# Kernel tuning notes

Hardware: AMD Instinct MI355X
Metric: run time of the kernel (lower is better)

## Reference

```python
import jax, jax.numpy as jnp
import numpy as np

EMB = 512      # emb_s * head_cnt = 64 * 8
EMB_S = 64     # scale uses sqrt(emb_s), not sqrt(emb) (quirk of source)
FF = 4 * EMB
LN_EPS = 1e-5


def layer_norm(x, g, b):
    mu = jnp.mean(x, axis=-1, keepdims=True)
    var = jnp.var(x, axis=-1, keepdims=True)
    return (x - mu) * jax.lax.rsqrt(var + LN_EPS) * g + b


def setup_inputs() -> dict:
    key = jax.random.key(0)
    ks = jax.random.split(key, 12)
    B, T = 512, 128
    s = 1.0 / np.sqrt(EMB)
    sf = 1.0 / np.sqrt(FF)
    return {
        "x": jax.random.normal(ks[0], (B, T, EMB), dtype=jnp.float32),
        "wq": jax.random.normal(ks[1], (EMB, EMB), dtype=jnp.float32) * s,
        "bq": jnp.zeros((EMB,), jnp.float32),
        "wk": jax.random.normal(ks[2], (EMB, EMB), dtype=jnp.float32) * s,
        "bk": jnp.zeros((EMB,), jnp.float32),
        "wv": jax.random.normal(ks[3], (EMB, EMB), dtype=jnp.float32) * s,
        "bv": jnp.zeros((EMB,), jnp.float32),
        "g1": jnp.ones((EMB,), jnp.float32),
        "b1": jnp.zeros((EMB,), jnp.float32),
        "g2": jnp.ones((EMB,), jnp.float32),
        "b2": jnp.zeros((EMB,), jnp.float32),
        "w1": jax.random.normal(ks[4], (EMB, FF), dtype=jnp.float32) * s,
        "bm1": jnp.zeros((FF,), jnp.float32),
        "w2": jax.random.normal(ks[5], (FF, EMB), dtype=jnp.float32) * sf,
        "bm2": jnp.zeros((EMB,), jnp.float32),
    }


def reference(x, wq, bq, wk, bk, wv, bv, g1, b1, g2, b2, w1, bm1, w2, bm2):
    B, T, E = x.shape
    # --- attention sub-block (single-head over full emb, per source forward) ---
    h = layer_norm(x, g1, b1)
    q = h @ wq + bq          # [B,T,E]
    k = h @ wk + bk
    v = h @ wv + bv
    att = jnp.einsum("bte,bse->bts", q, k) * (1.0 / np.sqrt(EMB_S))
    causal = jnp.tril(jnp.ones((T, T), dtype=bool))
    att = jnp.where(causal[None, :, :], att, -jnp.inf)
    att = jax.nn.softmax(att, axis=-1)
    y = jnp.einsum("bts,bse->bte", att, v)
    x = x + y  # note: no output projection / dropout on the forward path
    # --- MLP sub-block (dropout is identity in eval) ---
    h2 = layer_norm(x, g2, b2)
    m = jax.nn.gelu(h2 @ w1 + bm1, approximate=False) @ w2 + bm2
    return x + m
```

## Files before the change

### kernel.cpp

```cpp
#include <hip/hip_runtime.h>
#include <hip/hip_bf16.h>
#include <math.h>

typedef __attribute__((ext_vector_type(8))) short s16x8;
typedef __attribute__((ext_vector_type(4))) float f32x4;

static __device__ __forceinline__ float b2f(unsigned short u) {
    union { unsigned int u; float f; } x; x.u = ((unsigned int)u) << 16; return x.f;
}
static __device__ __forceinline__ unsigned short f2b(float f) {
    __hip_bfloat16 h = __float2bfloat16(f);
    return *reinterpret_cast<unsigned short*>(&h);
}
static __device__ __forceinline__ float gelu_fast(float x) {
    float s = x * fmaf(x * x, 0.07135481242f, 1.5957691216f);
    float e = __expf(-s);
    return x * __builtin_amdgcn_rcpf(1.0f + e);
}
static __device__ __forceinline__ void gload16(void* lds, const void* g) {
    __builtin_amdgcn_global_load_lds(
        (const __attribute__((address_space(1))) unsigned int*)g,
        (__attribute__((address_space(3))) unsigned int*)lds, 16, 0, 0);
}

__global__ __launch_bounds__(256) void cvt_t_kernel(
    const float* __restrict__ W, unsigned short* __restrict__ Wt, int K, int N)
{
    __shared__ unsigned short tile[32][33];
    int n0 = blockIdx.x * 32, k0 = blockIdx.y * 32;
    int tx = threadIdx.x & 31, ty = threadIdx.x >> 5;
#pragma unroll
    for (int p = 0; p < 32; p += 8)
        tile[tx][ty + p] = f2b(W[(size_t)(k0 + ty + p) * N + n0 + tx]);
    __syncthreads();
#pragma unroll
    for (int p = 0; p < 32; p += 8)
        Wt[(size_t)(n0 + ty + p) * K + k0 + tx] = tile[ty + p][tx];
}

__global__ __launch_bounds__(256) void concat3_kernel(
    const float* __restrict__ a, const float* __restrict__ b,
    const float* __restrict__ c, float* __restrict__ o)
{
    int i = blockIdx.x * 256 + threadIdx.x;
    if (i < 512) { o[i] = a[i]; o[512 + i] = b[i]; o[1024 + i] = c[i]; }
}

__global__ __launch_bounds__(256) void ln_kernel(
    const float* __restrict__ x,
    const float* __restrict__ g,
    const float* __restrict__ b,
    unsigned short* __restrict__ out, int rows)
{
    int row  = blockIdx.x * 4 + (threadIdx.x >> 6);
    int lane = threadIdx.x & 63;
    if (row >= rows) return;
    const float* xr = x + (size_t)row * 512 + lane * 8;
    float4 d0 = *(const float4*)xr;
    float4 d1 = *(const float4*)(xr + 4);
    float v[8] = {d0.x, d0.y, d0.z, d0.w, d1.x, d1.y, d1.z, d1.w};
    float s = 0.f, ss = 0.f;
#pragma unroll
    for (int j = 0; j < 8; ++j) { s += v[j]; ss += v[j] * v[j]; }
#pragma unroll
    for (int o = 32; o > 0; o >>= 1) { s += __shfl_xor(s, o); ss += __shfl_xor(ss, o); }
    float mu   = s * (1.0f / 512.0f);
    float var  = ss * (1.0f / 512.0f) - mu * mu;
    var = fmaxf(var, 0.0f);
    float rstd = rsqrtf(var + 1e-5f);
    float4 g0 = *(const float4*)(g + lane * 8);
    float4 g1 = *(const float4*)(g + lane * 8 + 4);
    float4 b0 = *(const float4*)(b + lane * 8);
    float4 b1 = *(const float4*)(b + lane * 8 + 4);
    float gg[8] = {g0.x, g0.y, g0.z, g0.w, g1.x, g1.y, g1.z, g1.w};
    float bb[8] = {b0.x, b0.y, b0.z, b0.w, b1.x, b1.y, b1.z, b1.w};
    uint4 res; unsigned short* rs = (unsigned short*)&res;
#pragma unroll
    for (int j = 0; j < 8; ++j)
        rs[j] = f2b((v[j] - mu) * rstd * gg[j] + bb[j]);
    *(uint4*)(out + (size_t)row * 512 + lane * 8) = res;
}

__global__ __launch_bounds__(512, 4) void gemm_bt_kernel(
    const unsigned short* __restrict__ A,
    const unsigned short* __restrict__ Bt,
    const float* __restrict__ bias,
    const float* __restrict__ residual,
    void* __restrict__ Cv,
    int M, int N, int K, int act_gelu, int out_f32)
{
    __shared__ unsigned short LA[3][256][32];
    __shared__ unsigned short LB[3][128][32];

    const int tid  = threadIdx.x;
    const int w    = tid >> 6, lane = tid & 63;
    const int quad = lane >> 4, l16 = lane & 15;
    const int wm   = (w >> 1) * 64, wn = (w & 1) * 64;

    int bx = blockIdx.x, by = blockIdx.y;
    {
        int nwg = gridDim.x * gridDim.y;
        if ((nwg & 7) == 0) {
            int lid = by * gridDim.x + bx;
            int cpx = nwg >> 3;
            lid = (lid & 7) * cpx + (lid >> 3);
            bx = lid % gridDim.x;
            by = lid / gridDim.x;
        }
    }
    const int bm = by * 256, bn = bx * 128;

    const int srow = w * 16 + (lane >> 2);
    const int sg   = (lane & 3) ^ ((lane >> 3) & 3);
    const unsigned short* a_src = A  + (size_t)(bm + srow) * K + sg * 8;
    const unsigned short* b_src = Bt + (size_t)(bn + srow) * K + sg * 8;
    const size_t a_skip = (size_t)128 * K;

    const int axor = (quad ^ ((l16 >> 1) & 3)) * 8;

    f32x4 acc[4][4] = {};
    const int nt = K >> 5;

    auto STG = [&](int sb, int kt) {
        const int ko = kt << 5;
        gload16(&LA[sb][w * 16][0],       a_src + ko);
        gload16(&LA[sb][128 + w * 16][0], a_src + a_skip + ko);
        gload16(&LB[sb][w * 16][0],       b_src + ko);
    };

    STG(0, 0);
    STG(1, 1);
    asm volatile("s_waitcnt vmcnt(3)" ::: "memory");
    __builtin_amdgcn_s_barrier();

    int cur = 0, stg = 2;
    for (int t = 0; t < nt; ++t) {
        s16x8 a4[4], b4[4];
#pragma unroll
        for (int m = 0; m < 4; ++m)
            a4[m] = *(const s16x8*)&LA[cur][wm + m * 16 + l16][axor];
#pragma unroll
        for (int n = 0; n < 4; ++n)
            b4[n] = *(const s16x8*)&LB[cur][wn + n * 16 + l16][axor];

        STG(stg, (t + 2 < nt) ? t + 2 : 0);
        asm volatile("s_waitcnt vmcnt(3)" ::: "memory");
        __builtin_amdgcn_sched_barrier(0);
        __builtin_amdgcn_s_barrier();
        __builtin_amdgcn_sched_barrier(0);

        __builtin_amdgcn_s_setprio(1);
#pragma unroll
        for (int m = 0; m < 4; ++m)
#pragma unroll
            for (int n = 0; n < 4; ++n)
                acc[m][n] = __builtin_amdgcn_mfma_f32_16x16x32_bf16(a4[m], b4[n], acc[m][n], 0, 0, 0);
        __builtin_amdgcn_s_setprio(0);
        __builtin_amdgcn_sched_barrier(0);
        __builtin_amdgcn_s_barrier();

        cur = (cur == 2) ? 0 : cur + 1;
        stg = (stg == 2) ? 0 : stg + 1;
    }
    asm volatile("s_waitcnt vmcnt(0)" ::: "memory");

#pragma unroll
    for (int m = 0; m < 4; ++m) {
#pragma unroll
        for (int n = 0; n < 4; ++n) {
#pragma unroll
            for (int r = 0; r < 4; ++r) {
                int row = bm + wm + m * 16 + quad * 4 + r;
                int col = bn + wn + n * 16 + l16;
                float val = acc[m][n][r] + bias[col];
                if (act_gelu) val = gelu_fast(val);
                if (residual) val += residual[(size_t)row * N + col];
                if (out_f32) ((float*)Cv)[(size_t)row * N + col] = val;
                else ((unsigned short*)Cv)[(size_t)row * N + col] = f2b(val);
            }
        }
    }
}

__global__ __launch_bounds__(256) void attn_kernel(
    const unsigned short* __restrict__ qkv,
    const float* __restrict__ x,
    float* __restrict__ x2)
{
    __shared__ unsigned short Ps[128][128];
    __shared__ unsigned short Vs[64][128];

    int b = blockIdx.x;
    int tid = threadIdx.x;
    int wave = tid >> 6, lane = tid & 63;
    int quad = lane >> 4, l16 = lane & 15;
    const unsigned short* qb = qkv + (size_t)b * 128 * 1536;
    const size_t bo = (size_t)b * 128 * 512;

    f32x4 acc[2][8] = {};
    for (int e0 = 0; e0 < 512; e0 += 32) {
        s16x8 a0 = *(const s16x8*)(qb + (size_t)(wave * 32 + l16) * 1536 + e0 + quad * 8);
        s16x8 a1 = *(const s16x8*)(qb + (size_t)(wave * 32 + 16 + l16) * 1536 + e0 + quad * 8);
#pragma unroll
        for (int j = 0; j < 8; ++j) {
            s16x8 bf = *(const s16x8*)(qb + (size_t)(j * 16 + l16) * 1536 + 512 + e0 + quad * 8);
            acc[0][j] = __builtin_amdgcn_mfma_f32_16x16x32_bf16(a0, bf, acc[0][j], 0, 0, 0);
            acc[1][j] = __builtin_amdgcn_mfma_f32_16x16x32_bf16(a1, bf, acc[1][j], 0, 0, 0);
        }
    }

    const float NEG = -1e30f;
#pragma unroll
    for (int i = 0; i < 2; ++i) {
#pragma unroll
        for (int r = 0; r < 4; ++r) {
            int t = wave * 32 + i * 16 + quad * 4 + r;
            float m = NEG;
#pragma unroll
            for (int j = 0; j < 8; ++j) {
                int s_col = j * 16 + l16;
                float val = acc[i][j][r] * 0.125f;
                val = (s_col <= t) ? val : NEG;
                acc[i][j][r] = val;
                m = fmaxf(m, val);
            }
            for (int o = 1; o < 16; o <<= 1) m = fmaxf(m, __shfl_xor(m, o));
            float sm = 0.f;
#pragma unroll
            for (int j = 0; j < 8; ++j) {
                float e = __expf(acc[i][j][r] - m);
                acc[i][j][r] = e;
                sm += e;
            }
            for (int o = 1; o < 16; o <<= 1) sm += __shfl_xor(sm, o);
            float inv = 1.0f / sm;
#pragma unroll
            for (int j = 0; j < 8; ++j) {
                int g = (j * 2 + (l16 >> 3)) ^ (t & 7);
                Ps[t][g * 8 + (l16 & 7)] = f2b(acc[i][j][r] * inv);
            }
        }
    }
    __syncthreads();

    const float* xb = x + bo;
    float* ob = x2 + bo;
    for (int e0 = 0; e0 < 512; e0 += 64) {
        if (e0) __syncthreads();
#pragma unroll
        for (int p = 0; p < 4; ++p) {
            int s = (tid >> 3) + p * 32;
            int c = (tid & 7) * 8;
            uint4 d = *(const uint4*)(qb + (size_t)s * 1536 + 1024 + e0 + c);
            const unsigned short* dsv = (const unsigned short*)&d;
#pragma unroll
            for (int j = 0; j < 8; ++j) {
                int rr = c + j;
                int g = (s >> 3) ^ j ^ (tid & 7);
                Vs[rr][g * 8 + (s & 7)] = dsv[j];
            }
        }
        __syncthreads();

        f32x4 acc2[2][4] = {};
#pragma unroll
        for (int ks = 0; ks < 4; ++ks) {
            int gp = ((ks * 4 + quad) ^ (l16 & 7)) * 8;
            s16x8 a0 = *(const s16x8*)(&Ps[wave * 32 + l16][gp]);
            s16x8 a1 = *(const s16x8*)(&Ps[wave * 32 + 16 + l16][gp]);
#pragma unroll
            for (int n = 0; n < 4; ++n) {
                int gv = ((ks * 4 + quad) ^ (l16 & 7) ^ ((2 * n + (l16 >> 3)) & 7)) * 8;
                s16x8 bf = *(const s16x8*)(&Vs[n * 16 + l16][gv]);
                acc2[0][n] = __builtin_amdgcn_mfma_f32_16x16x32_bf16(a0, bf, acc2[0][n], 0, 0, 0);
                acc2[1][n] = __builtin_amdgcn_mfma_f32_16x16x32_bf16(a1, bf, acc2[1][n], 0, 0, 0);
            }
        }
#pragma unroll
        for (int i = 0; i < 2; ++i) {
#pragma unroll
            for (int n = 0; n < 4; ++n) {
#pragma unroll
                for (int r = 0; r < 4; ++r) {
                    int t = wave * 32 + i * 16 + quad * 4 + r;
                    int e = e0 + n * 16 + l16;
                    ob[(size_t)t * 512 + e] = acc2[i][n][r] + xb[(size_t)t * 512 + e];
                }
            }
        }
    }
}

extern "C" void kernel_launch(void* const* d_in, const int* in_sizes, int n_in,
                              void* d_out, int out_size, void* d_ws, size_t ws_size,
                              hipStream_t stream) {
    const float* x   = (const float*)d_in[0];
    const float* wq  = (const float*)d_in[1];
    const float* bq  = (const float*)d_in[2];
    const float* wk  = (const float*)d_in[3];
    const float* bk  = (const float*)d_in[4];
    const float* wv  = (const float*)d_in[5];
    const float* bv  = (const float*)d_in[6];
    const float* g1  = (const float*)d_in[7];
    const float* b1  = (const float*)d_in[8];
    const float* g2  = (const float*)d_in[9];
    const float* b2  = (const float*)d_in[10];
    const float* w1  = (const float*)d_in[11];
    const float* bm1 = (const float*)d_in[12];
    const float* w2  = (const float*)d_in[13];
    const float* bm2 = (const float*)d_in[14];
    float* out = (float*)d_out;

    const int BATCH = 512, T = 128;
    dim3 blk(256), blkg(512);

    unsigned short* wqt = (unsigned short*)d_ws;
    unsigned short* wkt = wqt + 262144;
    unsigned short* wvt = wkt + 262144;
    unsigned short* w1t = wvt + 262144;
    unsigned short* w2t = w1t + 1048576;
    float* bqkv = (float*)(w2t + 1048576);
    cvt_t_kernel<<<dim3(16, 16), blk, 0, stream>>>(wq, wqt, 512, 512);
    cvt_t_kernel<<<dim3(16, 16), blk, 0, stream>>>(wk, wkt, 512, 512);
    cvt_t_kernel<<<dim3(16, 16), blk, 0, stream>>>(wv, wvt, 512, 512);
    cvt_t_kernel<<<dim3(64, 16), blk, 0, stream>>>(w1, w1t, 512, 2048);
    cvt_t_kernel<<<dim3(16, 64), blk, 0, stream>>>(w2, w2t, 2048, 512);
    concat3_kernel<<<dim3(2), blk, 0, stream>>>(bq, bk, bv, bqkv);

    int C = 512;
    while (C > 8 && 5773312ull + (size_t)C * 917504ull > ws_size) C >>= 1;

    const int R = C * T;
    const size_t S = (size_t)R * 512;
    char* dyn = (char*)(bqkv + 1536);
    unsigned short* h   = (unsigned short*)dyn;
    float*          x2f = (float*)(dyn + S * 2);
    unsigned short* qkv = (unsigned short*)(dyn + S * 2 + S * 4);
    unsigned short* mff = qkv;

    for (int b0 = 0; b0 < BATCH; b0 += C) {
        const size_t off = (size_t)b0 * T * 512;
        ln_kernel<<<R / 4, blk, 0, stream>>>(x + off, g1, b1, h, R);
        gemm_bt_kernel<<<dim3(12, R / 256), blkg, 0, stream>>>(h, wqt, bqkv, nullptr, qkv, R, 1536, 512, 0, 0);
        attn_kernel<<<C, blk, 0, stream>>>(qkv, x + off, x2f);
        ln_kernel<<<R / 4, blk, 0, stream>>>(x2f, g2, b2, h, R);
        gemm_bt_kernel<<<dim3(16, R / 256), blkg, 0, stream>>>(h, w1t, bm1, nullptr, mff, R, 2048, 512, 1, 0);
        gemm_bt_kernel<<<dim3(4, R / 256), blkg, 0, stream>>>(mff, w2t, bm2, x2f, out + off, R, 512, 2048, 0, 1);
    }
}
```

Before: 1.024 ms.

## Double GEMM K-tile to 64 with single barrier per iteration

The GEMM kernel's K-step grows from 32 to 64. LDS tiles are resized and a new 8-way XOR swizzle is used to match. The main loop now waits and barriers once at the top, issues the next stage's loads, then runs two k-halves of MFMAs, dropping the trailing barrier. This halves the number of loop iterations and barriers and issues more loads per stage. The cost is double the LDS use (about 144KB), with launch bounds lowered from 4 to 2 blocks per SM, which reduces occupancy.

```diff
diff --git a/kernel.cpp b/kernel.cpp
--- a/kernel.cpp
+++ b/kernel.cpp
@@ -81,7 +81,8 @@
     *(uint4*)(out + (size_t)row * 512 + lane * 8) = res;
 }
 
-__global__ __launch_bounds__(512, 4) void gemm_bt_kernel(
+template<int TAG>
+__global__ __launch_bounds__(512, 2) void gemm_bt_kernel(
     const unsigned short* __restrict__ A,
     const unsigned short* __restrict__ Bt,
     const float* __restrict__ bias,
@@ -89,8 +90,8 @@
     void* __restrict__ Cv,
     int M, int N, int K, int act_gelu, int out_f32)
 {
-    __shared__ unsigned short LA[3][256][32];
-    __shared__ unsigned short LB[3][128][32];
+    __shared__ unsigned short LA[3][256][64];
+    __shared__ unsigned short LB[3][128][64];
 
     const int tid  = threadIdx.x;
     const int w    = tid >> 6, lane = tid & 63;
@@ -110,54 +111,53 @@
     }
     const int bm = by * 256, bn = bx * 128;
 
-    const int srow = w * 16 + (lane >> 2);
-    const int sg   = (lane & 3) ^ ((lane >> 3) & 3);
-    const unsigned short* a_src = A  + (size_t)(bm + srow) * K + sg * 8;
-    const unsigned short* b_src = Bt + (size_t)(bn + srow) * K + sg * 8;
-    const size_t a_skip = (size_t)128 * K;
-
-    const int axor = (quad ^ ((l16 >> 1) & 3)) * 8;
+    const int sg = (tid & 7) ^ ((tid >> 3) & 7);
+    const unsigned short* a_srcp = A  + (size_t)(bm + w * 8 + ((lane >> 3))) * K + sg * 8;
+    const unsigned short* b_srcp = Bt + (size_t)(bn + w * 8 + ((lane >> 3))) * K + sg * 8;
+    const size_t rs64 = (size_t)64 * K;
 
     f32x4 acc[4][4] = {};
-    const int nt = K >> 5;
+    const int nt = K >> 6;
 
     auto STG = [&](int sb, int kt) {
-        const int ko = kt << 5;
-        gload16(&LA[sb][w * 16][0],       a_src + ko);
-        gload16(&LA[sb][128 + w * 16][0], a_src + a_skip + ko);
-        gload16(&LB[sb][w * 16][0],       b_src + ko);
+        const int ko = kt << 6;
+#pragma unroll
+        for (int c = 0; c < 4; ++c)
+            gload16(&LA[sb][c * 64 + w * 8][0], a_srcp + c * rs64 + ko);
+#pragma unroll
+        for (int c = 0; c < 2; ++c)
+            gload16(&LB[sb][c * 64 + w * 8][0], b_srcp + c * rs64 + ko);
     };
 
     STG(0, 0);
     STG(1, 1);
-    asm volatile("s_waitcnt vmcnt(3)" ::: "memory");
-    __builtin_amdgcn_s_barrier();
 
     int cur = 0, stg = 2;
     for (int t = 0; t < nt; ++t) {
-        s16x8 a4[4], b4[4];
-#pragma unroll
-        for (int m = 0; m < 4; ++m)
-            a4[m] = *(const s16x8*)&LA[cur][wm + m * 16 + l16][axor];
-#pragma unroll
-        for (int n = 0; n < 4; ++n)
-            b4[n] = *(const s16x8*)&LB[cur][wn + n * 16 + l16][axor];
-
-        STG(stg, (t + 2 < nt) ? t + 2 : 0);
-        asm volatile("s_waitcnt vmcnt(3)" ::: "memory");
-        __builtin_amdgcn_sched_barrier(0);
+        asm volatile("s_waitcnt vmcnt(6)" ::: "memory");
         __builtin_amdgcn_s_barrier();
         __builtin_amdgcn_sched_barrier(0);
 
-        __builtin_amdgcn_s_setprio(1);
-#pragma unroll
-        for (int m = 0; m < 4; ++m)
+        STG(stg, (t + 2 < nt) ? t + 2 : 0);
+
+#pragma unroll
+        for (int kh = 0; kh < 2; ++kh) {
+            s16x8 a4[4], b4[4];
+            const int gx = kh * 4 + quad;
+#pragma unroll
+            for (int m = 0; m < 4; ++m)
+                a4[m] = *(const s16x8*)&LA[cur][wm + m * 16 + l16][(gx ^ (l16 & 7)) * 8];
 #pragma unroll
             for (int n = 0; n < 4; ++n)
-                acc[m][n] = __builtin_amdgcn_mfma_f32_16x16x32_bf16(a4[m], b4[n], acc[m][n], 0, 0, 0);
-        __builtin_amdgcn_s_setprio(0);
-        __builtin_amdgcn_sched_barrier(0);
-        __builtin_amdgcn_s_barrier();
+                b4[n] = *(const s16x8*)&LB[cur][wn + n * 16 + l16][(gx ^ (l16 & 7)) * 8];
+            __builtin_amdgcn_s_setprio(1);
+#pragma unroll
+            for (int m = 0; m < 4; ++m)
+#pragma unroll
+                for (int n = 0; n < 4; ++n)
+                    acc[m][n] = __builtin_amdgcn_mfma_f32_16x16x32_bf16(a4[m], b4[n], acc[m][n], 0, 0, 0);
+            __builtin_amdgcn_s_setprio(0);
+        }
 
         cur = (cur == 2) ? 0 : cur + 1;
         stg = (stg == 2) ? 0 : stg + 1;
@@ -341,10 +341,10 @@
     for (int b0 = 0; b0 < BATCH; b0 += C) {
         const size_t off = (size_t)b0 * T * 512;
         ln_kernel<<<R / 4, blk, 0, stream>>>(x + off, g1, b1, h, R);
-        gemm_bt_kernel<<<dim3(12, R / 256), blkg, 0, stream>>>(h, wqt, bqkv, nullptr, qkv, R, 1536, 512, 0, 0);
+        gemm_bt_kernel<0><<<dim3(12, R / 256), blkg, 0, stream>>>(h, wqt, bqkv, nullptr, qkv, R, 1536, 512, 0, 0);
         attn_kernel<<<C, blk, 0, stream>>>(qkv, x + off, x2f);
         ln_kernel<<<R / 4, blk, 0, stream>>>(x2f, g2, b2, h, R);
-        gemm_bt_kernel<<<dim3(16, R / 256), blkg, 0, stream>>>(h, w1t, bm1, nullptr, mff, R, 2048, 512, 1, 0);
-        gemm_bt_kernel<<<dim3(4, R / 256), blkg, 0, stream>>>(mff, w2t, bm2, x2f, out + off, R, 512, 2048, 0, 1);
-    }
-}
+        gemm_bt_kernel<1><<<dim3(16, R / 256), blkg, 0, stream>>>(h, w1t, bm1, nullptr, mff, R, 2048, 512, 1, 0);
+        gemm_bt_kernel<2><<<dim3(4, R / 256), blkg, 0, stream>>>(mff, w2t, bm2, x2f, out + off, R, 512, 2048, 0, 1);
+    }
+}
```

Measured after the change: 1.297 ms. 1.27x slower.
